# Optimization experiments

Hardware: AMD Instinct MI355X
Metric: run time of the kernel (lower is better)

## Reference

```python
import jax, jax.numpy as jnp
import numpy as np

BN_EPS = 1e-5

def binarize_ste(x):
    # sign() in forward; identity (straight-through) in backward, matching the
    # weight.data / input.data hack in BinarizeConv2d.
    return x + jax.lax.stop_gradient(jnp.sign(x) - x)


def setup_inputs() -> dict:
    key = jax.random.key(0)
    k1, k2, k3, k4 = jax.random.split(key, 4)
    N, Cin, H, W = 16, 32, 224, 224
    Cout, K = 32, 3
    x = jax.random.normal(k1, (N, Cin, H, W), dtype=jnp.float32)
    weight = jax.random.normal(k2, (Cout, Cin, K, K), dtype=jnp.float32) * 0.1
    gamma = jax.random.uniform(k3, (Cout,), dtype=jnp.float32, minval=0.5, maxval=1.5)
    beta = jax.random.normal(k4, (Cout,), dtype=jnp.float32) * 0.1
    return {"x": x, "weight": weight, "gamma": gamma, "beta": beta}


def reference(x, weight, gamma, beta):
    # BinarizeConv2d: binarize input iff C != 3, always binarize weights.
    xb = binarize_ste(x) if x.shape[1] != 3 else x
    wb = binarize_ste(weight)
    y = jax.lax.conv_general_dilated(
        xb, wb,
        window_strides=(1, 1),
        padding=((1, 1), (1, 1)),
        dimension_numbers=("NCHW", "OIHW", "NCHW"),
    )  # [N, Cout, H, W]
    # BatchNorm2d in training mode: per-channel batch statistics over (N, H, W).
    mean = jnp.mean(y, axis=(0, 2, 3))
    var = jnp.var(y, axis=(0, 2, 3))
    inv = jax.lax.rsqrt(var + BN_EPS)
    yn = (y - mean[None, :, None, None]) * inv[None, :, None, None]
    return yn * gamma[None, :, None, None] + beta[None, :, None, None]
```

## Files before the change

kernel.cpp:

```cpp
#include <hip/hip_runtime.h>
#include <stdint.h>

#define NB 16
#define CC 32
#define HH 224
#define WWID 224
#define HWS (HH*WWID)
#define NHWT (NB*HWS)
#define STRIPS (NHWT/4)
#define SPI (HWS/4)
#define SPR (WWID/4)

#define PITCH 232
#define PROWS 226
#define IMGW (PITCH*PROWS)

typedef float    f4 __attribute__((ext_vector_type(4)));
typedef unsigned u4 __attribute__((ext_vector_type(4)));
typedef unsigned u2 __attribute__((ext_vector_type(2)));

#define WS_WSIGN 0
#define WS_WNZ   2048
#define WS_BASE  4096
#define WS_FLAGW 5248
#define WS_FLAGZ 5252
#define WS_SSUM  5376
#define WS_SSQ   5632
#define WS_SCALE 5888
#define WS_SHIFT 6016
#define WS_XS    8192
#define WS_XNZ   (8192 + (size_t)NB*IMGW*4)

__global__ void pack_w(const float* __restrict__ w, unsigned* __restrict__ wsg,
                       unsigned* __restrict__ wnz, int* __restrict__ flagw,
                       int* __restrict__ baset, int* __restrict__ s_sum,
                       unsigned long long* __restrict__ s_sq, int* __restrict__ flagz) {
    __shared__ unsigned s_sg[288];
    __shared__ int allnz;
    if (threadIdx.x == 0) { allnz = 1; *flagz = 0; }
    if (threadIdx.x < CC) { s_sum[threadIdx.x] = 0; s_sq[threadIdx.x] = 0ull; }
    __syncthreads();
    int k = threadIdx.x;
    if (k < 288) {
        int co = k / 9, tap = k % 9;
        unsigned bits = 0, nz = 0;
        for (int ci = 0; ci < CC; ++ci) {
            float v = w[(co * CC + ci) * 9 + tap];
            bits |= (v > 0.f ? 1u : 0u) << ci;
            nz   |= (v != 0.f ? 1u : 0u) << ci;
        }
        wsg[k] = bits; wnz[k] = nz; s_sg[k] = bits;
        if (nz != 0xffffffffu) atomicAnd(&allnz, 0);
    }
    __syncthreads();
    if (threadIdx.x == 0) *flagw = allnz;
    if (k < 288) {
        int cls = k >> 5, co = k & 31;
        int hc = cls / 3, wc = cls % 3;
        int nv = 0, corr = 0;
        #pragma unroll
        for (int kh = 0; kh < 3; ++kh)
            #pragma unroll
            for (int kw = 0; kw < 3; ++kw) {
                bool inv = (hc == 0 && kh == 0) || (hc == 2 && kh == 2) ||
                           (wc == 0 && kw == 0) || (wc == 2 && kw == 2);
                if (inv) corr += __popc(s_sg[co * 9 + kh * 3 + kw]);
                else     nv++;
            }
        baset[k] = 32 * nv + 2 * corr;
    }
}

__global__ void __launch_bounds__(256) pack_x4(const float* __restrict__ x,
                                               unsigned* __restrict__ xs,
                                               unsigned* __restrict__ xnz,
                                               int* __restrict__ flagz) {
    int t = blockIdx.x * 256 + threadIdx.x;
    int n = t / SPI, rem = t - n * SPI;
    int h = rem / SPR, w0 = (rem - h * SPR) * 4;
    const float* base = x + (size_t)n * CC * HWS + h * WWID + w0;
    unsigned b0=0,b1=0,b2=0,b3=0, z0=0,z1=0,z2=0,z3=0;
    #pragma unroll
    for (int c = 0; c < CC; ++c) {
        f4 v = __builtin_nontemporal_load((const f4*)(base + (size_t)c * HWS));
        b0 |= (v.x > 0.f ? (1u<<c) : 0u);  z0 |= (v.x != 0.f ? (1u<<c) : 0u);
        b1 |= (v.y > 0.f ? (1u<<c) : 0u);  z1 |= (v.y != 0.f ? (1u<<c) : 0u);
        b2 |= (v.z > 0.f ? (1u<<c) : 0u);  z2 |= (v.z != 0.f ? (1u<<c) : 0u);
        b3 |= (v.w > 0.f ? (1u<<c) : 0u);  z3 |= (v.w != 0.f ? (1u<<c) : 0u);
    }
    size_t rowb = (size_t)n * IMGW + (h + 1) * PITCH;
    size_t d = rowb + 1 + w0;
    xs[d+0]=b0; xs[d+1]=b1; xs[d+2]=b2; xs[d+3]=b3;
    xnz[d+0]=z0; xnz[d+1]=z1; xnz[d+2]=z2; xnz[d+3]=z3;

    if (w0 == 0)        { xs[rowb] = 0;       xnz[rowb] = 0; }
    if (w0 == WWID - 4) { xs[rowb + 225] = 0; xnz[rowb + 225] = 0; }
    if (h == 0) {
        size_t tr = (size_t)n * IMGW;
        #pragma unroll
        for (int j = 0; j < 4; ++j) { xs[tr + 1 + w0 + j] = 0; xnz[tr + 1 + w0 + j] = 0; }
        if (w0 == 0)        { xs[tr] = 0;       xnz[tr] = 0; }
        if (w0 == WWID - 4) { xs[tr + 225] = 0; xnz[tr + 225] = 0; }
    }
    if (h == HH - 1) {
        size_t br = (size_t)n * IMGW + (size_t)(PROWS - 1) * PITCH;
        #pragma unroll
        for (int j = 0; j < 4; ++j) { xs[br + 1 + w0 + j] = 0; xnz[br + 1 + w0 + j] = 0; }
        if (w0 == 0)        { xs[br] = 0;       xnz[br] = 0; }
        if (w0 == WWID - 4) { xs[br + 225] = 0; xnz[br + 225] = 0; }
    }

    bool hasz = (z0 & z1 & z2 & z3) != 0xffffffffu;
    if (__any(hasz) && (threadIdx.x & 63) == 0) atomicOr(flagz, 1);
}

__device__ __forceinline__ void loadwin(const unsigned* __restrict__ p, unsigned a[6]) {
    u4 lo = *(const u4*)p;
    u2 hi = *(const u2*)(p + 4);
    a[0]=lo.x; a[1]=lo.y; a[2]=lo.z; a[3]=lo.w; a[4]=hi.x; a[5]=hi.y;
}

__device__ __forceinline__ void ad4(const unsigned a0[6], const unsigned a1[6],
                                    const unsigned a2[6],
                                    const unsigned* __restrict__ q, int ad[4]) {
    unsigned q0=q[0],q1=q[1],q2=q[2],q3=q[3],q4=q[4],q5=q[5],q6=q[6],q7=q[7],q8=q[8];
    #pragma unroll
    for (int px = 0; px < 4; ++px) {
        ad[px] = __popc(a0[px]^q0) + __popc(a0[px+1]^q1) + __popc(a0[px+2]^q2)
               + __popc(a1[px]^q3) + __popc(a1[px+1]^q4) + __popc(a1[px+2]^q5)
               + __popc(a2[px]^q6) + __popc(a2[px+1]^q7) + __popc(a2[px+2]^q8);
    }
}

__device__ __forceinline__ void y4_slowc(const unsigned a0[6], const unsigned a1[6],
                                         const unsigned a2[6], const unsigned z0[6],
                                         const unsigned z1[6], const unsigned z2[6],
                                         const unsigned* __restrict__ qs,
                                         const unsigned* __restrict__ qz, int y[4]) {
    #pragma unroll
    for (int px = 0; px < 4; ++px) {
        int am = 0, ad = 0;
        #pragma unroll
        for (int kw = 0; kw < 3; ++kw) {
            unsigned m0 = z0[px+kw] & qz[kw];
            unsigned m1 = z1[px+kw] & qz[3+kw];
            unsigned m2 = z2[px+kw] & qz[6+kw];
            am += __popc(m0) + __popc(m1) + __popc(m2);
            ad += __popc((a0[px+kw]^qs[kw])   & m0)
                + __popc((a1[px+kw]^qs[3+kw]) & m1)
                + __popc((a2[px+kw]^qs[6+kw]) & m2);
        }
        y[px] = am - 2 * ad;
    }
}

__global__ void __launch_bounds__(256, 8) convstats(
        const unsigned* __restrict__ xs, const unsigned* __restrict__ xnz,
        const unsigned* __restrict__ wsg, const unsigned* __restrict__ wnz,
        const int* __restrict__ baset, const int* __restrict__ flagw,
        const int* __restrict__ flagz, int* __restrict__ s_sum,
        unsigned long long* __restrict__ s_sq) {
    __shared__ int sb[288];
    __shared__ int ls[4][8], lq[4][8];
    for (int i = threadIdx.x; i < 288; i += 256) sb[i] = baset[i];
    __syncthreads();

    int cobase = (blockIdx.x & 3) * 8;
    int sid = (blockIdx.x >> 2) * 256 + threadIdx.x;
    int n = sid / SPI, rem = sid - n * SPI;
    int h = rem / SPR, w0 = (rem - h * SPR) * 4;
    size_t off = (size_t)n * IMGW + h * PITCH + w0;

    unsigned a0[6], a1[6], a2[6];
    loadwin(xs + off, a0); loadwin(xs + off + PITCH, a1); loadwin(xs + off + 2*PITCH, a2);

    int sacc[8], qacc[8];
    bool fast = (*flagw != 0) && (*flagz == 0);
    if (fast) {
        int hc = (h == 0) ? 0 : ((h == HH-1) ? 6 : 3);
        int c0 = (hc + ((w0 == 0) ? 0 : 1)) * 32;
        int c1 = (hc + 1) * 32;
        int c3 = (hc + ((w0 == WWID-4) ? 2 : 1)) * 32;
        #pragma unroll
        for (int u = 0; u < 8; ++u) {
            int co = cobase + u;
            int ad[4];
            ad4(a0, a1, a2, wsg + co * 9, ad);
            int y0 = sb[c0 + co] - 2 * ad[0];
            int y1 = sb[c1 + co] - 2 * ad[1];
            int y2 = sb[c1 + co] - 2 * ad[2];
            int y3 = sb[c3 + co] - 2 * ad[3];
            sacc[u] = y0 + y1 + y2 + y3;
            qacc[u] = y0*y0 + y1*y1 + y2*y2 + y3*y3;
        }
    } else {
        unsigned z0[6], z1[6], z2[6];
        loadwin(xnz + off, z0); loadwin(xnz + off + PITCH, z1); loadwin(xnz + off + 2*PITCH, z2);
        #pragma unroll
        for (int u = 0; u < 8; ++u) {
            int co = cobase + u;
            int y[4];
            y4_slowc(a0, a1, a2, z0, z1, z2, wsg + co * 9, wnz + co * 9, y);
            sacc[u] = y[0]+y[1]+y[2]+y[3];
            qacc[u] = y[0]*y[0]+y[1]*y[1]+y[2]*y[2]+y[3]*y[3];
        }
    }

    #pragma unroll
    for (int off2 = 32; off2; off2 >>= 1) {
        #pragma unroll
        for (int u = 0; u < 8; ++u) {
            sacc[u] += __shfl_down(sacc[u], off2);
            qacc[u] += __shfl_down(qacc[u], off2);
        }
    }
    int wid = threadIdx.x >> 6, lane = threadIdx.x & 63;
    if (lane == 0) {
        #pragma unroll
        for (int u = 0; u < 8; ++u) { ls[wid][u] = sacc[u]; lq[wid][u] = qacc[u]; }
    }
    __syncthreads();
    if (threadIdx.x < 8) {
        int u = threadIdx.x;
        int S = ls[0][u] + ls[1][u] + ls[2][u] + ls[3][u];
        long long Q = (long long)lq[0][u] + lq[1][u] + lq[2][u] + lq[3][u];
        atomicAdd(&s_sum[cobase + u], S);
        atomicAdd(&s_sq[cobase + u], (unsigned long long)Q);
    }
}

__global__ void bfinal(const int* __restrict__ s_sum,
                       const unsigned long long* __restrict__ s_sq,
                       const float* __restrict__ gamma, const float* __restrict__ beta,
                       float* __restrict__ scale, float* __restrict__ shift) {
    int c = threadIdx.x;
    if (c >= CC) return;
    double mean = (double)s_sum[c] / (double)NHWT;
    double var  = (double)(long long)s_sq[c] / (double)NHWT - mean * mean;
    float inv = (float)(1.0 / sqrt(var + 1e-5));
    float g = gamma[c] * inv;
    scale[c] = g;
    shift[c] = beta[c] - (float)mean * g;
}

__global__ void __launch_bounds__(256, 8) convnorm(
        const unsigned* __restrict__ xs, const unsigned* __restrict__ xnz,
        const unsigned* __restrict__ wsg, const unsigned* __restrict__ wnz,
        const int* __restrict__ baset, const int* __restrict__ flagw,
        const int* __restrict__ flagz, const float* __restrict__ scale,
        const float* __restrict__ shift, float* __restrict__ out) {
    __shared__ int sb[288];
    for (int i = threadIdx.x; i < 288; i += 256) sb[i] = baset[i];
    __syncthreads();

    int cobase = (blockIdx.x & 3) * 8;
    int sid = (blockIdx.x >> 2) * 256 + threadIdx.x;
    int n = sid / SPI, rem = sid - n * SPI;
    int h = rem / SPR, w0 = (rem - h * SPR) * 4;
    size_t off = (size_t)n * IMGW + h * PITCH + w0;

    unsigned a0[6], a1[6], a2[6];
    loadwin(xs + off, a0); loadwin(xs + off + PITCH, a1); loadwin(xs + off + 2*PITCH, a2);

    float* on = out + (size_t)(n * CC + cobase) * HWS + h * WWID + w0;
    bool fast = (*flagw != 0) && (*flagz == 0);
    if (fast) {
        int hc = (h == 0) ? 0 : ((h == HH-1) ? 6 : 3);
        int c0 = (hc + ((w0 == 0) ? 0 : 1)) * 32;
        int c1 = (hc + 1) * 32;
        int c3 = (hc + ((w0 == WWID-4) ? 2 : 1)) * 32;
        #pragma unroll
        for (int u = 0; u < 8; ++u) {
            int co = cobase + u;
            int ad[4];
            ad4(a0, a1, a2, wsg + co * 9, ad);
            int y0 = sb[c0 + co] - 2 * ad[0];
            int y1 = sb[c1 + co] - 2 * ad[1];
            int y2 = sb[c1 + co] - 2 * ad[2];
            int y3 = sb[c3 + co] - 2 * ad[3];
            float sc = scale[co], sh = shift[co];
            f4 o = { fmaf((float)y0, sc, sh), fmaf((float)y1, sc, sh),
                     fmaf((float)y2, sc, sh), fmaf((float)y3, sc, sh) };
            __builtin_nontemporal_store(o, (f4*)(on + (size_t)u * HWS));
        }
    } else {
        unsigned z0[6], z1[6], z2[6];
        loadwin(xnz + off, z0); loadwin(xnz + off + PITCH, z1); loadwin(xnz + off + 2*PITCH, z2);
        #pragma unroll
        for (int u = 0; u < 8; ++u) {
            int co = cobase + u;
            int y[4];
            y4_slowc(a0, a1, a2, z0, z1, z2, wsg + co * 9, wnz + co * 9, y);
            float sc = scale[co], sh = shift[co];
            f4 o = { fmaf((float)y[0], sc, sh), fmaf((float)y[1], sc, sh),
                     fmaf((float)y[2], sc, sh), fmaf((float)y[3], sc, sh) };
            __builtin_nontemporal_store(o, (f4*)(on + (size_t)u * HWS));
        }
    }
}

extern "C" void kernel_launch(void* const* d_in, const int* in_sizes, int n_in,
                              void* d_out, int out_size, void* d_ws, size_t ws_size,
                              hipStream_t stream) {
    const float* x     = (const float*)d_in[0];
    const float* w     = (const float*)d_in[1];
    const float* gamma = (const float*)d_in[2];
    const float* beta  = (const float*)d_in[3];
    float* out = (float*)d_out;

    char* ws = (char*)d_ws;
    unsigned* wsg            = (unsigned*)(ws + WS_WSIGN);
    unsigned* wnz            = (unsigned*)(ws + WS_WNZ);
    int* baset               = (int*)(ws + WS_BASE);
    int* flagw               = (int*)(ws + WS_FLAGW);
    int* flagz               = (int*)(ws + WS_FLAGZ);
    int* s_sum               = (int*)(ws + WS_SSUM);
    unsigned long long* s_sq = (unsigned long long*)(ws + WS_SSQ);
    float* scale             = (float*)(ws + WS_SCALE);
    float* shift             = (float*)(ws + WS_SHIFT);
    unsigned* xsb            = (unsigned*)(ws + WS_XS);
    unsigned* xzb            = (unsigned*)(ws + WS_XNZ);

    int cgrid = STRIPS / 256 * 4;
    pack_w   <<<1, 320, 0, stream>>>(w, wsg, wnz, flagw, baset, s_sum, s_sq, flagz);
    pack_x4  <<<STRIPS / 256, 256, 0, stream>>>(x, xsb, xzb, flagz);
    convstats<<<cgrid, 256, 0, stream>>>(xsb, xzb, wsg, wnz, baset, flagw, flagz, s_sum, s_sq);
    bfinal   <<<1, 64, 0, stream>>>(s_sum, s_sq, gamma, beta, scale, shift);
    convnorm <<<cgrid, 256, 0, stream>>>(xsb, xzb, wsg, wnz, baset, flagw, flagz,
                                         scale, shift, out);
}
```

Baseline: 84.50 us.

## Widen conv strips to eight pixels and fold small kernels into neighbors

Each thread in the conv stats and conv norm passes now computes eight output pixels instead of four. This reuses the loaded 3-row bit window across more outputs and halves the grid. The weight-packing kernel is merged into the input-packing kernel via block 0, and a memset replaces the zero-initialisation it used to do. The BN finalisation kernel is folded into the prologue of the normalise kernel, which cuts the number of launches from five to three. In exchange, register pressure rises (launch bounds drop from 8 to 6) and every normalise block redundantly recomputes scale and shift.

```diff
diff --git a/kernel.cpp b/kernel.cpp
--- a/kernel.cpp
+++ b/kernel.cpp
@@ -10,6 +10,9 @@
 #define STRIPS (NHWT/4)
 #define SPI (HWS/4)
 #define SPR (WWID/4)
+#define PAIRS (NHWT/8)
+#define PPI (HWS/8)
+#define PPR (WWID/8)
 
 #define PITCH 232
 #define PROWS 226
@@ -26,55 +29,50 @@
 #define WS_FLAGZ 5252
 #define WS_SSUM  5376
 #define WS_SSQ   5632
-#define WS_SCALE 5888
-#define WS_SHIFT 6016
 #define WS_XS    8192
 #define WS_XNZ   (8192 + (size_t)NB*IMGW*4)
 
-__global__ void pack_w(const float* __restrict__ w, unsigned* __restrict__ wsg,
-                       unsigned* __restrict__ wnz, int* __restrict__ flagw,
-                       int* __restrict__ baset, int* __restrict__ s_sum,
-                       unsigned long long* __restrict__ s_sq, int* __restrict__ flagz) {
+__global__ void __launch_bounds__(256) pack_x4(
+        const float* __restrict__ x, const float* __restrict__ w,
+        unsigned* __restrict__ xs, unsigned* __restrict__ xnz,
+        unsigned* __restrict__ wsg, unsigned* __restrict__ wnz,
+        int* __restrict__ flagw, int* __restrict__ flagz, int* __restrict__ baset) {
     __shared__ unsigned s_sg[288];
     __shared__ int allnz;
-    if (threadIdx.x == 0) { allnz = 1; *flagz = 0; }
-    if (threadIdx.x < CC) { s_sum[threadIdx.x] = 0; s_sq[threadIdx.x] = 0ull; }
-    __syncthreads();
-    int k = threadIdx.x;
-    if (k < 288) {
-        int co = k / 9, tap = k % 9;
-        unsigned bits = 0, nz = 0;
-        for (int ci = 0; ci < CC; ++ci) {
-            float v = w[(co * CC + ci) * 9 + tap];
-            bits |= (v > 0.f ? 1u : 0u) << ci;
-            nz   |= (v != 0.f ? 1u : 0u) << ci;
-        }
-        wsg[k] = bits; wnz[k] = nz; s_sg[k] = bits;
-        if (nz != 0xffffffffu) atomicAnd(&allnz, 0);
-    }
-    __syncthreads();
-    if (threadIdx.x == 0) *flagw = allnz;
-    if (k < 288) {
-        int cls = k >> 5, co = k & 31;
-        int hc = cls / 3, wc = cls % 3;
-        int nv = 0, corr = 0;
-        #pragma unroll
-        for (int kh = 0; kh < 3; ++kh)
-            #pragma unroll
-            for (int kw = 0; kw < 3; ++kw) {
-                bool inv = (hc == 0 && kh == 0) || (hc == 2 && kh == 2) ||
-                           (wc == 0 && kw == 0) || (wc == 2 && kw == 2);
-                if (inv) corr += __popc(s_sg[co * 9 + kh * 3 + kw]);
-                else     nv++;
-            }
-        baset[k] = 32 * nv + 2 * corr;
-    }
-}
-
-__global__ void __launch_bounds__(256) pack_x4(const float* __restrict__ x,
-                                               unsigned* __restrict__ xs,
-                                               unsigned* __restrict__ xnz,
-                                               int* __restrict__ flagz) {
+
+    if (blockIdx.x == 0) {
+        if (threadIdx.x == 0) allnz = 1;
+        __syncthreads();
+        for (int k = threadIdx.x; k < 288; k += 256) {
+            int co = k / 9, tap = k % 9;
+            unsigned bits = 0, nz = 0;
+            for (int ci = 0; ci < CC; ++ci) {
+                float v = w[(co * CC + ci) * 9 + tap];
+                bits |= (v > 0.f ? 1u : 0u) << ci;
+                nz   |= (v != 0.f ? 1u : 0u) << ci;
+            }
+            wsg[k] = bits; wnz[k] = nz; s_sg[k] = bits;
+            if (nz != 0xffffffffu) atomicAnd(&allnz, 0);
+        }
+        __syncthreads();
+        if (threadIdx.x == 0) *flagw = allnz;
+        for (int k = threadIdx.x; k < 288; k += 256) {
+            int cls = k >> 5, co = k & 31;
+            int hc = cls / 3, wc = cls % 3;
+            int nv = 0, corr = 0;
+            #pragma unroll
+            for (int kh = 0; kh < 3; ++kh)
+                #pragma unroll
+                for (int kw = 0; kw < 3; ++kw) {
+                    bool inv = (hc == 0 && kh == 0) || (hc == 2 && kh == 2) ||
+                               (wc == 0 && kw == 0) || (wc == 2 && kw == 2);
+                    if (inv) corr += __popc(s_sg[co * 9 + kh * 3 + kw]);
+                    else     nv++;
+                }
+            baset[k] = 32 * nv + 2 * corr;
+        }
+    }
+
     int t = blockIdx.x * 256 + threadIdx.x;
     int n = t / SPI, rem = t - n * SPI;
     int h = rem / SPR, w0 = (rem - h * SPR) * 4;
@@ -114,47 +112,21 @@
     if (__any(hasz) && (threadIdx.x & 63) == 0) atomicOr(flagz, 1);
 }
 
-__device__ __forceinline__ void loadwin(const unsigned* __restrict__ p, unsigned a[6]) {
+__device__ __forceinline__ void loadwin10(const unsigned* __restrict__ p, unsigned a[10]) {
+    u4 lo  = *(const u4*)p;
+    u4 mid = *(const u4*)(p + 4);
+    u2 hi  = *(const u2*)(p + 8);
+    a[0]=lo.x; a[1]=lo.y; a[2]=lo.z; a[3]=lo.w;
+    a[4]=mid.x; a[5]=mid.y; a[6]=mid.z; a[7]=mid.w;
+    a[8]=hi.x; a[9]=hi.y;
+}
+__device__ __forceinline__ void loadwin6(const unsigned* __restrict__ p, unsigned a[6]) {
     u4 lo = *(const u4*)p;
     u2 hi = *(const u2*)(p + 4);
     a[0]=lo.x; a[1]=lo.y; a[2]=lo.z; a[3]=lo.w; a[4]=hi.x; a[5]=hi.y;
 }
 
-__device__ __forceinline__ void ad4(const unsigned a0[6], const unsigned a1[6],
-                                    const unsigned a2[6],
-                                    const unsigned* __restrict__ q, int ad[4]) {
-    unsigned q0=q[0],q1=q[1],q2=q[2],q3=q[3],q4=q[4],q5=q[5],q6=q[6],q7=q[7],q8=q[8];
-    #pragma unroll
-    for (int px = 0; px < 4; ++px) {
-        ad[px] = __popc(a0[px]^q0) + __popc(a0[px+1]^q1) + __popc(a0[px+2]^q2)
-               + __popc(a1[px]^q3) + __popc(a1[px+1]^q4) + __popc(a1[px+2]^q5)
-               + __popc(a2[px]^q6) + __popc(a2[px+1]^q7) + __popc(a2[px+2]^q8);
-    }
-}
-
-__device__ __forceinline__ void y4_slowc(const unsigned a0[6], const unsigned a1[6],
-                                         const unsigned a2[6], const unsigned z0[6],
-                                         const unsigned z1[6], const unsigned z2[6],
-                                         const unsigned* __restrict__ qs,
-                                         const unsigned* __restrict__ qz, int y[4]) {
-    #pragma unroll
-    for (int px = 0; px < 4; ++px) {
-        int am = 0, ad = 0;
-        #pragma unroll
-        for (int kw = 0; kw < 3; ++kw) {
-            unsigned m0 = z0[px+kw] & qz[kw];
-            unsigned m1 = z1[px+kw] & qz[3+kw];
-            unsigned m2 = z2[px+kw] & qz[6+kw];
-            am += __popc(m0) + __popc(m1) + __popc(m2);
-            ad += __popc((a0[px+kw]^qs[kw])   & m0)
-                + __popc((a1[px+kw]^qs[3+kw]) & m1)
-                + __popc((a2[px+kw]^qs[6+kw]) & m2);
-        }
-        y[px] = am - 2 * ad;
-    }
-}
-
-__global__ void __launch_bounds__(256, 8) convstats(
+__global__ void __launch_bounds__(256, 6) convstats(
         const unsigned* __restrict__ xs, const unsigned* __restrict__ xnz,
         const unsigned* __restrict__ wsg, const unsigned* __restrict__ wnz,
         const int* __restrict__ baset, const int* __restrict__ flagw,
@@ -166,52 +138,78 @@
     __syncthreads();
 
     int cobase = (blockIdx.x & 3) * 8;
-    int sid = (blockIdx.x >> 2) * 256 + threadIdx.x;
-    int n = sid / SPI, rem = sid - n * SPI;
-    int h = rem / SPR, w0 = (rem - h * SPR) * 4;
+    int pid = (blockIdx.x >> 2) * 256 + threadIdx.x;
+    int n = pid / PPI, rem = pid - n * PPI;
+    int h = rem / PPR, w0 = (rem - h * PPR) * 8;
     size_t off = (size_t)n * IMGW + h * PITCH + w0;
 
-    unsigned a0[6], a1[6], a2[6];
-    loadwin(xs + off, a0); loadwin(xs + off + PITCH, a1); loadwin(xs + off + 2*PITCH, a2);
+    unsigned a0[10], a1[10], a2[10];
+    loadwin10(xs + off, a0); loadwin10(xs + off + PITCH, a1); loadwin10(xs + off + 2*PITCH, a2);
 
     int sacc[8], qacc[8];
+    #pragma unroll
+    for (int u = 0; u < 8; ++u) { sacc[u] = 0; qacc[u] = 0; }
+
     bool fast = (*flagw != 0) && (*flagz == 0);
     if (fast) {
         int hc = (h == 0) ? 0 : ((h == HH-1) ? 6 : 3);
-        int c0 = (hc + ((w0 == 0) ? 0 : 1)) * 32;
-        int c1 = (hc + 1) * 32;
-        int c3 = (hc + ((w0 == WWID-4) ? 2 : 1)) * 32;
+        int cbL = (hc + ((w0 == 0) ? 0 : 1)) * 32;
+        int cbM = (hc + 1) * 32;
+        int cbR = (hc + ((w0 == WWID-8) ? 2 : 1)) * 32;
         #pragma unroll
         for (int u = 0; u < 8; ++u) {
             int co = cobase + u;
-            int ad[4];
-            ad4(a0, a1, a2, wsg + co * 9, ad);
-            int y0 = sb[c0 + co] - 2 * ad[0];
-            int y1 = sb[c1 + co] - 2 * ad[1];
-            int y2 = sb[c1 + co] - 2 * ad[2];
-            int y3 = sb[c3 + co] - 2 * ad[3];
-            sacc[u] = y0 + y1 + y2 + y3;
-            qacc[u] = y0*y0 + y1*y1 + y2*y2 + y3*y3;
+            const unsigned* q = wsg + co * 9;
+            unsigned q0=q[0],q1=q[1],q2=q[2],q3=q[3],q4=q[4],q5=q[5],q6=q[6],q7=q[7],q8=q[8];
+            int bL = sb[cbL + co], bM = sb[cbM + co], bR = sb[cbR + co];
+            #pragma unroll
+            for (int p = 0; p < 8; ++p) {
+                int t = __popc(a0[p]^q0) + __popc(a0[p+1]^q1) + __popc(a0[p+2]^q2)
+                      + __popc(a1[p]^q3) + __popc(a1[p+1]^q4) + __popc(a1[p+2]^q5)
+                      + __popc(a2[p]^q6) + __popc(a2[p+1]^q7) + __popc(a2[p+2]^q8);
+                int b = (p == 0) ? bL : ((p == 7) ? bR : bM);
+                int y = b - 2 * t;
+                sacc[u] += y; qacc[u] += y * y;
+            }
         }
     } else {
-        unsigned z0[6], z1[6], z2[6];
-        loadwin(xnz + off, z0); loadwin(xnz + off + PITCH, z1); loadwin(xnz + off + 2*PITCH, z2);
+        #pragma unroll
+        for (int half = 0; half < 2; ++half) {
+            unsigned z0[6], z1[6], z2[6];
+            loadwin6(xnz + off + half*4, z0);
+            loadwin6(xnz + off + PITCH + half*4, z1);
+            loadwin6(xnz + off + 2*PITCH + half*4, z2);
+            #pragma unroll
+            for (int u = 0; u < 8; ++u) {
+                int co = cobase + u;
+                const unsigned* qs = wsg + co * 9;
+                const unsigned* qz = wnz + co * 9;
+                #pragma unroll
+                for (int p = 0; p < 4; ++p) {
+                    int am = 0, ad = 0;
+                    #pragma unroll
+                    for (int kw = 0; kw < 3; ++kw) {
+                        unsigned m0 = z0[p+kw] & qz[kw];
+                        unsigned m1 = z1[p+kw] & qz[3+kw];
+                        unsigned m2 = z2[p+kw] & qz[6+kw];
+                        am += __popc(m0) + __popc(m1) + __popc(m2);
+                        ad += __popc((a0[half*4+p+kw]^qs[kw])   & m0)
+                            + __popc((a1[half*4+p+kw]^qs[3+kw]) & m1)
+                            + __popc((a2[half*4+p+kw]^qs[6+kw]) & m2);
+                    }
+                    int y = am - 2 * ad;
+                    sacc[u] += y; qacc[u] += y * y;
+                }
+            }
+        }
+    }
+
+    #pragma unroll
+    for (int o2 = 32; o2; o2 >>= 1) {
         #pragma unroll
         for (int u = 0; u < 8; ++u) {
-            int co = cobase + u;
-            int y[4];
-            y4_slowc(a0, a1, a2, z0, z1, z2, wsg + co * 9, wnz + co * 9, y);
-            sacc[u] = y[0]+y[1]+y[2]+y[3];
-            qacc[u] = y[0]*y[0]+y[1]*y[1]+y[2]*y[2]+y[3]*y[3];
-        }
-    }
-
-    #pragma unroll
-    for (int off2 = 32; off2; off2 >>= 1) {
-        #pragma unroll
-        for (int u = 0; u < 8; ++u) {
-            sacc[u] += __shfl_down(sacc[u], off2);
-            qacc[u] += __shfl_down(qacc[u], off2);
+            sacc[u] += __shfl_down(sacc[u], o2);
+            qacc[u] += __shfl_down(qacc[u], o2);
         }
     }
     int wid = threadIdx.x >> 6, lane = threadIdx.x & 63;
@@ -229,72 +227,95 @@
     }
 }
 
-__global__ void bfinal(const int* __restrict__ s_sum,
-                       const unsigned long long* __restrict__ s_sq,
-                       const float* __restrict__ gamma, const float* __restrict__ beta,
-                       float* __restrict__ scale, float* __restrict__ shift) {
-    int c = threadIdx.x;
-    if (c >= CC) return;
-    double mean = (double)s_sum[c] / (double)NHWT;
-    double var  = (double)(long long)s_sq[c] / (double)NHWT - mean * mean;
-    float inv = (float)(1.0 / sqrt(var + 1e-5));
-    float g = gamma[c] * inv;
-    scale[c] = g;
-    shift[c] = beta[c] - (float)mean * g;
-}
-
-__global__ void __launch_bounds__(256, 8) convnorm(
+__global__ void __launch_bounds__(256, 6) convnorm(
         const unsigned* __restrict__ xs, const unsigned* __restrict__ xnz,
         const unsigned* __restrict__ wsg, const unsigned* __restrict__ wnz,
         const int* __restrict__ baset, const int* __restrict__ flagw,
-        const int* __restrict__ flagz, const float* __restrict__ scale,
-        const float* __restrict__ shift, float* __restrict__ out) {
+        const int* __restrict__ flagz, const int* __restrict__ s_sum,
+        const unsigned long long* __restrict__ s_sq,
+        const float* __restrict__ gamma, const float* __restrict__ beta,
+        float* __restrict__ out) {
     __shared__ int sb[288];
+    __shared__ float s_sc[32], s_sh[32];
     for (int i = threadIdx.x; i < 288; i += 256) sb[i] = baset[i];
+    if (threadIdx.x < 32) {
+        int c = threadIdx.x;
+        double mean = (double)s_sum[c] / (double)NHWT;
+        double var  = (double)(long long)s_sq[c] / (double)NHWT - mean * mean;
+        float inv = (float)(1.0 / sqrt(var + 1e-5));
+        float g = gamma[c] * inv;
+        s_sc[c] = g;
+        s_sh[c] = beta[c] - (float)mean * g;
+    }
     __syncthreads();
 
     int cobase = (blockIdx.x & 3) * 8;
-    int sid = (blockIdx.x >> 2) * 256 + threadIdx.x;
-    int n = sid / SPI, rem = sid - n * SPI;
-    int h = rem / SPR, w0 = (rem - h * SPR) * 4;
+    int pid = (blockIdx.x >> 2) * 256 + threadIdx.x;
+    int n = pid / PPI, rem = pid - n * PPI;
+    int h = rem / PPR, w0 = (rem - h * PPR) * 8;
     size_t off = (size_t)n * IMGW + h * PITCH + w0;
 
-    unsigned a0[6], a1[6], a2[6];
-    loadwin(xs + off, a0); loadwin(xs + off + PITCH, a1); loadwin(xs + off + 2*PITCH, a2);
+    unsigned a0[10], a1[10], a2[10];
+    loadwin10(xs + off, a0); loadwin10(xs + off + PITCH, a1); loadwin10(xs + off + 2*PITCH, a2);
 
     float* on = out + (size_t)(n * CC + cobase) * HWS + h * WWID + w0;
     bool fast = (*flagw != 0) && (*flagz == 0);
     if (fast) {
         int hc = (h == 0) ? 0 : ((h == HH-1) ? 6 : 3);
-        int c0 = (hc + ((w0 == 0) ? 0 : 1)) * 32;
-        int c1 = (hc + 1) * 32;
-        int c3 = (hc + ((w0 == WWID-4) ? 2 : 1)) * 32;
+        int cbL = (hc + ((w0 == 0) ? 0 : 1)) * 32;
+        int cbM = (hc + 1) * 32;
+        int cbR = (hc + ((w0 == WWID-8) ? 2 : 1)) * 32;
         #pragma unroll
         for (int u = 0; u < 8; ++u) {
             int co = cobase + u;
-            int ad[4];
-            ad4(a0, a1, a2, wsg + co * 9, ad);
-            int y0 = sb[c0 + co] - 2 * ad[0];
-            int y1 = sb[c1 + co] - 2 * ad[1];
-            int y2 = sb[c1 + co] - 2 * ad[2];
-            int y3 = sb[c3 + co] - 2 * ad[3];
-            float sc = scale[co], sh = shift[co];
-            f4 o = { fmaf((float)y0, sc, sh), fmaf((float)y1, sc, sh),
-                     fmaf((float)y2, sc, sh), fmaf((float)y3, sc, sh) };
-            __builtin_nontemporal_store(o, (f4*)(on + (size_t)u * HWS));
+            const unsigned* q = wsg + co * 9;
+            unsigned q0=q[0],q1=q[1],q2=q[2],q3=q[3],q4=q[4],q5=q[5],q6=q[6],q7=q[7],q8=q[8];
+            int bL = sb[cbL + co], bM = sb[cbM + co], bR = sb[cbR + co];
+            float sc = s_sc[co], sh = s_sh[co];
+            f4 o0, o1;
+            #pragma unroll
+            for (int p = 0; p < 8; ++p) {
+                int t = __popc(a0[p]^q0) + __popc(a0[p+1]^q1) + __popc(a0[p+2]^q2)
+                      + __popc(a1[p]^q3) + __popc(a1[p+1]^q4) + __popc(a1[p+2]^q5)
+                      + __popc(a2[p]^q6) + __popc(a2[p+1]^q7) + __popc(a2[p+2]^q8);
+                int b = (p == 0) ? bL : ((p == 7) ? bR : bM);
+                float ov = fmaf((float)(b - 2*t), sc, sh);
+                if (p < 4) o0[p] = ov; else o1[p-4] = ov;
+            }
+            __builtin_nontemporal_store(o0, (f4*)(on + (size_t)u * HWS));
+            __builtin_nontemporal_store(o1, (f4*)(on + (size_t)u * HWS + 4));
         }
     } else {
-        unsigned z0[6], z1[6], z2[6];
-        loadwin(xnz + off, z0); loadwin(xnz + off + PITCH, z1); loadwin(xnz + off + 2*PITCH, z2);
-        #pragma unroll
-        for (int u = 0; u < 8; ++u) {
-            int co = cobase + u;
-            int y[4];
-            y4_slowc(a0, a1, a2, z0, z1, z2, wsg + co * 9, wnz + co * 9, y);
-            float sc = scale[co], sh = shift[co];
-            f4 o = { fmaf((float)y[0], sc, sh), fmaf((float)y[1], sc, sh),
-                     fmaf((float)y[2], sc, sh), fmaf((float)y[3], sc, sh) };
-            __builtin_nontemporal_store(o, (f4*)(on + (size_t)u * HWS));
+        #pragma unroll
+        for (int half = 0; half < 2; ++half) {
+            unsigned z0[6], z1[6], z2[6];
+            loadwin6(xnz + off + half*4, z0);
+            loadwin6(xnz + off + PITCH + half*4, z1);
+            loadwin6(xnz + off + 2*PITCH + half*4, z2);
+            #pragma unroll
+            for (int u = 0; u < 8; ++u) {
+                int co = cobase + u;
+                const unsigned* qs = wsg + co * 9;
+                const unsigned* qz = wnz + co * 9;
+                float sc = s_sc[co], sh = s_sh[co];
+                f4 o;
+                #pragma unroll
+                for (int p = 0; p < 4; ++p) {
+                    int am = 0, ad = 0;
+                    #pragma unroll
+                    for (int kw = 0; kw < 3; ++kw) {
+                        unsigned m0 = z0[p+kw] & qz[kw];
+                        unsigned m1 = z1[p+kw] & qz[3+kw];
+                        unsigned m2 = z2[p+kw] & qz[6+kw];
+                        am += __popc(m0) + __popc(m1) + __popc(m2);
+                        ad += __popc((a0[half*4+p+kw]^qs[kw])   & m0)
+                            + __popc((a1[half*4+p+kw]^qs[3+kw]) & m1)
+                            + __popc((a2[half*4+p+kw]^qs[6+kw]) & m2);
+                    }
+                    o[p] = fmaf((float)(am - 2*ad), sc, sh);
+                }
+                __builtin_nontemporal_store(o, (f4*)(on + (size_t)u * HWS + half*4));
+            }
         }
     }
 }
@@ -316,16 +337,16 @@
     int* flagz               = (int*)(ws + WS_FLAGZ);
     int* s_sum               = (int*)(ws + WS_SSUM);
     unsigned long long* s_sq = (unsigned long long*)(ws + WS_SSQ);
-    float* scale             = (float*)(ws + WS_SCALE);
-    float* shift             = (float*)(ws + WS_SHIFT);
     unsigned* xsb            = (unsigned*)(ws + WS_XS);
     unsigned* xzb            = (unsigned*)(ws + WS_XNZ);
 
-    int cgrid = STRIPS / 256 * 4;
-    pack_w   <<<1, 320, 0, stream>>>(w, wsg, wnz, flagw, baset, s_sum, s_sq, flagz);
-    pack_x4  <<<STRIPS / 256, 256, 0, stream>>>(x, xsb, xzb, flagz);
-    convstats<<<cgrid, 256, 0, stream>>>(xsb, xzb, wsg, wnz, baset, flagw, flagz, s_sum, s_sq);
-    bfinal   <<<1, 64, 0, stream>>>(s_sum, s_sq, gamma, beta, scale, shift);
+    hipMemsetAsync(ws + WS_FLAGW, 0, 640, stream);
+
+    int cgrid = PAIRS / 256 * 4;
+    pack_x4  <<<STRIPS / 256, 256, 0, stream>>>(x, w, xsb, xzb, wsg, wnz,
+                                                flagw, flagz, baset);
+    convstats<<<cgrid, 256, 0, stream>>>(xsb, xzb, wsg, wnz, baset, flagw, flagz,
+                                         s_sum, s_sq);
     convnorm <<<cgrid, 256, 0, stream>>>(xsb, xzb, wsg, wnz, baset, flagw, flagz,
-                                         scale, shift, out);
-}
+                                         s_sum, s_sq, gamma, beta, out);
+}
```

Result: slower. 107.7 us (+27.5%).

## Fold weight packing into pack_x4 and BN finalize into convnorm

Applied to the files above, without the earlier changes.

Weight packing moves into block 0 of the input-packing kernel, and per-channel scale/shift are now computed by every convnorm block into shared memory. This removes two tiny kernel launches. The flag and stat buffers are zeroed with a memset instead. Output stores change from nontemporal to regular. In exchange, every convnorm block does redundant double-precision finalize work and block 0 of pack_x4 runs longer.

```diff
diff --git a/kernel.cpp b/kernel.cpp
--- a/kernel.cpp
+++ b/kernel.cpp
@@ -26,55 +26,50 @@
 #define WS_FLAGZ 5252
 #define WS_SSUM  5376
 #define WS_SSQ   5632
-#define WS_SCALE 5888
-#define WS_SHIFT 6016
 #define WS_XS    8192
 #define WS_XNZ   (8192 + (size_t)NB*IMGW*4)
 
-__global__ void pack_w(const float* __restrict__ w, unsigned* __restrict__ wsg,
-                       unsigned* __restrict__ wnz, int* __restrict__ flagw,
-                       int* __restrict__ baset, int* __restrict__ s_sum,
-                       unsigned long long* __restrict__ s_sq, int* __restrict__ flagz) {
+__global__ void __launch_bounds__(256) pack_x4(
+        const float* __restrict__ x, const float* __restrict__ w,
+        unsigned* __restrict__ xs, unsigned* __restrict__ xnz,
+        unsigned* __restrict__ wsg, unsigned* __restrict__ wnz,
+        int* __restrict__ flagw, int* __restrict__ flagz, int* __restrict__ baset) {
     __shared__ unsigned s_sg[288];
     __shared__ int allnz;
-    if (threadIdx.x == 0) { allnz = 1; *flagz = 0; }
-    if (threadIdx.x < CC) { s_sum[threadIdx.x] = 0; s_sq[threadIdx.x] = 0ull; }
-    __syncthreads();
-    int k = threadIdx.x;
-    if (k < 288) {
-        int co = k / 9, tap = k % 9;
-        unsigned bits = 0, nz = 0;
-        for (int ci = 0; ci < CC; ++ci) {
-            float v = w[(co * CC + ci) * 9 + tap];
-            bits |= (v > 0.f ? 1u : 0u) << ci;
-            nz   |= (v != 0.f ? 1u : 0u) << ci;
-        }
-        wsg[k] = bits; wnz[k] = nz; s_sg[k] = bits;
-        if (nz != 0xffffffffu) atomicAnd(&allnz, 0);
-    }
-    __syncthreads();
-    if (threadIdx.x == 0) *flagw = allnz;
-    if (k < 288) {
-        int cls = k >> 5, co = k & 31;
-        int hc = cls / 3, wc = cls % 3;
-        int nv = 0, corr = 0;
-        #pragma unroll
-        for (int kh = 0; kh < 3; ++kh)
+
+    if (blockIdx.x == 0) {
+        if (threadIdx.x == 0) allnz = 1;
+        __syncthreads();
+        for (int k = threadIdx.x; k < 288; k += 256) {
+            int co = k / 9, tap = k % 9;
+            unsigned bits = 0, nz = 0;
+            for (int ci = 0; ci < CC; ++ci) {
+                float v = w[(co * CC + ci) * 9 + tap];
+                bits |= (v > 0.f ? 1u : 0u) << ci;
+                nz   |= (v != 0.f ? 1u : 0u) << ci;
+            }
+            wsg[k] = bits; wnz[k] = nz; s_sg[k] = bits;
+            if (nz != 0xffffffffu) atomicAnd(&allnz, 0);
+        }
+        __syncthreads();
+        if (threadIdx.x == 0) *flagw = allnz;
+        for (int k = threadIdx.x; k < 288; k += 256) {
+            int cls = k >> 5, co = k & 31;
+            int hc = cls / 3, wc = cls % 3;
+            int nv = 0, corr = 0;
             #pragma unroll
-            for (int kw = 0; kw < 3; ++kw) {
-                bool inv = (hc == 0 && kh == 0) || (hc == 2 && kh == 2) ||
-                           (wc == 0 && kw == 0) || (wc == 2 && kw == 2);
-                if (inv) corr += __popc(s_sg[co * 9 + kh * 3 + kw]);
-                else     nv++;
-            }
-        baset[k] = 32 * nv + 2 * corr;
-    }
-}
-
-__global__ void __launch_bounds__(256) pack_x4(const float* __restrict__ x,
-                                               unsigned* __restrict__ xs,
-                                               unsigned* __restrict__ xnz,
-                                               int* __restrict__ flagz) {
+            for (int kh = 0; kh < 3; ++kh)
+                #pragma unroll
+                for (int kw = 0; kw < 3; ++kw) {
+                    bool inv = (hc == 0 && kh == 0) || (hc == 2 && kh == 2) ||
+                               (wc == 0 && kw == 0) || (wc == 2 && kw == 2);
+                    if (inv) corr += __popc(s_sg[co * 9 + kh * 3 + kw]);
+                    else     nv++;
+                }
+            baset[k] = 32 * nv + 2 * corr;
+        }
+    }
+
     int t = blockIdx.x * 256 + threadIdx.x;
     int n = t / SPI, rem = t - n * SPI;
     int h = rem / SPR, w0 = (rem - h * SPR) * 4;
@@ -207,11 +202,11 @@
     }
 
     #pragma unroll
-    for (int off2 = 32; off2; off2 >>= 1) {
-        #pragma unroll
-        for (int u = 0; u < 8; ++u) {
-            sacc[u] += __shfl_down(sacc[u], off2);
-            qacc[u] += __shfl_down(qacc[u], off2);
+    for (int o2 = 32; o2; o2 >>= 1) {
+        #pragma unroll
+        for (int u = 0; u < 8; ++u) {
+            sacc[u] += __shfl_down(sacc[u], o2);
+            qacc[u] += __shfl_down(qacc[u], o2);
         }
     }
     int wid = threadIdx.x >> 6, lane = threadIdx.x & 63;
@@ -229,28 +224,26 @@
     }
 }
 
-__global__ void bfinal(const int* __restrict__ s_sum,
-                       const unsigned long long* __restrict__ s_sq,
-                       const float* __restrict__ gamma, const float* __restrict__ beta,
-                       float* __restrict__ scale, float* __restrict__ shift) {
-    int c = threadIdx.x;
-    if (c >= CC) return;
-    double mean = (double)s_sum[c] / (double)NHWT;
-    double var  = (double)(long long)s_sq[c] / (double)NHWT - mean * mean;
-    float inv = (float)(1.0 / sqrt(var + 1e-5));
-    float g = gamma[c] * inv;
-    scale[c] = g;
-    shift[c] = beta[c] - (float)mean * g;
-}
-
 __global__ void __launch_bounds__(256, 8) convnorm(
         const unsigned* __restrict__ xs, const unsigned* __restrict__ xnz,
         const unsigned* __restrict__ wsg, const unsigned* __restrict__ wnz,
         const int* __restrict__ baset, const int* __restrict__ flagw,
-        const int* __restrict__ flagz, const float* __restrict__ scale,
-        const float* __restrict__ shift, float* __restrict__ out) {
+        const int* __restrict__ flagz, const int* __restrict__ s_sum,
+        const unsigned long long* __restrict__ s_sq,
+        const float* __restrict__ gamma, const float* __restrict__ beta,
+        float* __restrict__ out) {
     __shared__ int sb[288];
+    __shared__ float s_sc[32], s_sh[32];
     for (int i = threadIdx.x; i < 288; i += 256) sb[i] = baset[i];
+    if (threadIdx.x < 32) {
+        int c = threadIdx.x;
+        double mean = (double)s_sum[c] / (double)NHWT;
+        double var  = (double)(long long)s_sq[c] / (double)NHWT - mean * mean;
+        float inv = (float)(1.0 / sqrt(var + 1e-5));
+        float g = gamma[c] * inv;
+        s_sc[c] = g;
+        s_sh[c] = beta[c] - (float)mean * g;
+    }
     __syncthreads();
 
     int cobase = (blockIdx.x & 3) * 8;
@@ -278,10 +271,10 @@
             int y1 = sb[c1 + co] - 2 * ad[1];
             int y2 = sb[c1 + co] - 2 * ad[2];
             int y3 = sb[c3 + co] - 2 * ad[3];
-            float sc = scale[co], sh = shift[co];
+            float sc = s_sc[co], sh = s_sh[co];
             f4 o = { fmaf((float)y0, sc, sh), fmaf((float)y1, sc, sh),
                      fmaf((float)y2, sc, sh), fmaf((float)y3, sc, sh) };
-            __builtin_nontemporal_store(o, (f4*)(on + (size_t)u * HWS));
+            *(f4*)(on + (size_t)u * HWS) = o;
         }
     } else {
         unsigned z0[6], z1[6], z2[6];
@@ -291,10 +284,10 @@
             int co = cobase + u;
             int y[4];
             y4_slowc(a0, a1, a2, z0, z1, z2, wsg + co * 9, wnz + co * 9, y);
-            float sc = scale[co], sh = shift[co];
+            float sc = s_sc[co], sh = s_sh[co];
             f4 o = { fmaf((float)y[0], sc, sh), fmaf((float)y[1], sc, sh),
                      fmaf((float)y[2], sc, sh), fmaf((float)y[3], sc, sh) };
-            __builtin_nontemporal_store(o, (f4*)(on + (size_t)u * HWS));
+            *(f4*)(on + (size_t)u * HWS) = o;
         }
     }
 }
@@ -316,16 +309,16 @@
     int* flagz               = (int*)(ws + WS_FLAGZ);
     int* s_sum               = (int*)(ws + WS_SSUM);
     unsigned long long* s_sq = (unsigned long long*)(ws + WS_SSQ);
-    float* scale             = (float*)(ws + WS_SCALE);
-    float* shift             = (float*)(ws + WS_SHIFT);
     unsigned* xsb            = (unsigned*)(ws + WS_XS);
     unsigned* xzb            = (unsigned*)(ws + WS_XNZ);
 
+    hipMemsetAsync(ws + WS_FLAGW, 0, 640, stream);
+
     int cgrid = STRIPS / 256 * 4;
-    pack_w   <<<1, 320, 0, stream>>>(w, wsg, wnz, flagw, baset, s_sum, s_sq, flagz);
-    pack_x4  <<<STRIPS / 256, 256, 0, stream>>>(x, xsb, xzb, flagz);
-    convstats<<<cgrid, 256, 0, stream>>>(xsb, xzb, wsg, wnz, baset, flagw, flagz, s_sum, s_sq);
-    bfinal   <<<1, 64, 0, stream>>>(s_sum, s_sq, gamma, beta, scale, shift);
+    pack_x4  <<<STRIPS / 256, 256, 0, stream>>>(x, w, xsb, xzb, wsg, wnz,
+                                                flagw, flagz, baset);
+    convstats<<<cgrid, 256, 0, stream>>>(xsb, xzb, wsg, wnz, baset, flagw, flagz,
+                                         s_sum, s_sq);
     convnorm <<<cgrid, 256, 0, stream>>>(xsb, xzb, wsg, wnz, baset, flagw, flagz,
-                                         scale, shift, out);
-}
+                                         s_sum, s_sq, gamma, beta, out);
+}
```

New measurement: 81.23 us. -3.9%, faster.
